# Kernel tuning notes

Measured on AMD Instinct MI355X. Metric: run time of the kernel, lower is better.

## Reference

```python
import jax, jax.numpy as jnp
import numpy as np

B, C, T, F = 64, 128, 2048, 5
ALPHA, BETA = 0.5, 0.5
N = C * F  # 640 nodes


def _spatial_adjacency():
    # |i-j| <= 3 neighbors within each frequency band block (block diagonal)
    idx = np.arange(C)
    d = np.abs(idx[:, None] - idx[None, :])
    blk = ((d <= 3) & (d > 0)).astype(np.float32)
    return jnp.asarray(np.kron(np.eye(F, dtype=np.float32), blk))


A_SPATIAL = _spatial_adjacency()  # (N, N)


def setup_inputs() -> dict:
    key = jax.random.key(0)
    ks = jax.random.split(key, 5)
    names = ['delta', 'theta', 'alpha', 'beta', 'gamma']
    return {n: jax.random.normal(k, (B, C, T), dtype=jnp.float32) for n, k in zip(names, ks)}


def _strg(delta, theta, alpha, beta, gamma):
    bands = jnp.stack([delta, theta, alpha, beta, gamma], axis=1)  # (B, F, C, T)
    Bn, Fn, Cn, Tn = bands.shape

    # bandpower = unbiased variance over time (torch.var default ddof=1)
    bp = jnp.var(bands, axis=3, ddof=1)  # (B, F, C)
    bandpowers = jnp.transpose(bp, (0, 2, 1))  # (B, C, F)
    # node ordering: node f*C + ch -> bandpowers[b, ch, f] == bp[b, f, ch]
    node_features = bp.reshape(Bn, Fn * Cn, 1)

    # Pearson-style functional connectivity per batch & band (vectorized)
    mean = jnp.mean(bands, axis=3, keepdims=True)
    std = jnp.std(bands, axis=3, ddof=1, keepdims=True)  # torch.std unbiased
    xn = (bands - mean) / (std + 1e-8)
    corr = jnp.einsum('bfct,bfdt->bfcd', xn, xn) / (Tn - 1)  # (B, F, C, C)
    corr = jnp.abs(corr)
    eye = jnp.eye(Cn, dtype=corr.dtype)
    corr = corr * (1.0 - eye) + eye  # zero diag, then set diag = 1
    corr = 0.5 * (corr + jnp.swapaxes(corr, 2, 3))

    # block-diagonal assembly into full functional adjacency
    A_func = jnp.zeros((Bn, N, N), dtype=corr.dtype)
    for f in range(Fn):
        s = f * Cn
        A_func = A_func.at[:, s:s + Cn, s:s + Cn].set(corr[:, f])

    A = ALPHA * A_SPATIAL[None] + BETA * A_func  # (B, N, N)

    # symmetric degree normalization D^-1/2 A D^-1/2
    D = jnp.sum(A, axis=2)
    d_inv_sqrt = (D + 1e-8) ** -0.5
    d_inv_sqrt = jnp.where(jnp.isinf(d_inv_sqrt), 0.0, d_inv_sqrt)
    A_norm = d_inv_sqrt[:, :, None] * A * d_inv_sqrt[:, None, :]

    return A_norm, node_features, bandpowers


def reference(delta, theta, alpha, beta, gamma):
    return _strg(delta, theta, alpha, beta, gamma)
```

## Files before the change

kernel.cpp:

```cpp
#include <hip/hip_runtime.h>
#include <hip/hip_bf16.h>

#define Bn 64
#define Cn 128
#define Tn 2048
#define Fn 5
#define Nn 640
#define TCHUNK 64
#define NCHUNK 32
#define BUFBYTES (Cn * TCHUNK * 2)

typedef __attribute__((ext_vector_type(8))) short bf16x8;
typedef __attribute__((ext_vector_type(4))) short bf16x4;
typedef __attribute__((ext_vector_type(4))) float f32x4;

__device__ __forceinline__ short f2bf(float f) {
    union { float f; unsigned u; } v; v.f = f;
    unsigned r = (v.u + 0x7fffu + ((v.u >> 16) & 1u)) >> 16;
    return (short)r;
}

__device__ __forceinline__ int swz(int row, int bytecol) {
    return (row * 128 + bytecol) ^ ((row & 7) << 4);
}

__device__ __forceinline__ const float* pick_band(const float* d0, const float* d1,
                                                  const float* d2, const float* d3,
                                                  const float* d4, int f) {
    return (f == 0) ? d0 : (f == 1) ? d1 : (f == 2) ? d2 : (f == 3) ? d3 : d4;
}

__global__ __launch_bounds__(512, 4)
void strg_mono(const float* __restrict__ d0, const float* __restrict__ d1,
               const float* __restrict__ d2, const float* __restrict__ d3,
               const float* __restrict__ d4, float* __restrict__ out)
{
    __shared__ __align__(16) char smem[Cn * Cn * 4];
    __shared__ float S_lds[Cn], diag[Cn], mrow[Cn], ivrow[Cn], Dsum[Cn], dinv_s[Cn];

    const int tid = threadIdx.x;
    const int bfid = blockIdx.x;
    const int b = bfid / Fn;
    const int f = bfid - b * Fn;
    const float* src = pick_band(d0, d1, d2, d3, d4, f) + (size_t)b * Cn * Tn;

    if (tid < Cn) { S_lds[tid] = 0.0f; Dsum[tid] = 0.0f; }

    const int srow = tid >> 4;
    const int sseg = tid & 15;
    const float* tb0 = src + (size_t)srow * Tn + sseg * 4;

    const int lane = tid & 63;
    const int w  = tid >> 6;
    const int wr = w >> 1;
    const int wc = w & 1;
    const int r0 = wr * 32;
    const int c0 = wc * 64;
    const int lg = lane >> 4;
    const int ll = lane & 15;

    f32x4 acc[2][4] = {};
    float psum[4] = {0.f, 0.f, 0.f, 0.f};
    float4 pfA[4], pfB[4];

    auto issueA = [&](int ch) {
        const float* cb = tb0 + ch * TCHUNK;
        #pragma unroll
        for (int i = 0; i < 4; ++i) pfA[i] = *(const float4*)(cb + (size_t)(i * 32) * Tn);
    };
    auto issueB = [&](int ch) {
        const float* cb = tb0 + ch * TCHUNK;
        #pragma unroll
        for (int i = 0; i < 4; ++i) pfB[i] = *(const float4*)(cb + (size_t)(i * 32) * Tn);
    };
    auto convA = [&](int buf) {
        char* base = smem + buf * BUFBYTES;
        #pragma unroll
        for (int i = 0; i < 4; ++i) {
            const int row = i * 32 + srow;
            float4 v = pfA[i];
            psum[i] += v.x + v.y + v.z + v.w;
            bf16x4 h; h[0] = f2bf(v.x); h[1] = f2bf(v.y); h[2] = f2bf(v.z); h[3] = f2bf(v.w);
            *(bf16x4*)(base + swz(row, sseg * 8)) = h;
        }
    };
    auto convB = [&](int buf) {
        char* base = smem + buf * BUFBYTES;
        #pragma unroll
        for (int i = 0; i < 4; ++i) {
            const int row = i * 32 + srow;
            float4 v = pfB[i];
            psum[i] += v.x + v.y + v.z + v.w;
            bf16x4 h; h[0] = f2bf(v.x); h[1] = f2bf(v.y); h[2] = f2bf(v.z); h[3] = f2bf(v.w);
            *(bf16x4*)(base + swz(row, sseg * 8)) = h;
        }
    };
    auto mfma_phase = [&](int buf) {
        const char* base = smem + buf * BUFBYTES;
        #pragma unroll
        for (int ks = 0; ks < 2; ++ks) {
            bf16x8 afr[2], bfr[4];
            #pragma unroll
            for (int m = 0; m < 2; ++m)
                afr[m] = *(const bf16x8*)(base + swz(r0 + m * 16 + ll, ks * 64 + lg * 16));
            #pragma unroll
            for (int n = 0; n < 4; ++n)
                bfr[n] = *(const bf16x8*)(base + swz(c0 + n * 16 + ll, ks * 64 + lg * 16));
            #pragma unroll
            for (int m = 0; m < 2; ++m)
                #pragma unroll
                for (int n = 0; n < 4; ++n)
                    acc[m][n] = __builtin_amdgcn_mfma_f32_16x16x32_bf16(afr[m], bfr[n], acc[m][n], 0, 0, 0);
        }
    };

    issueA(0);
    issueB(1);
    convA(0);
    issueA(2);
    asm volatile("s_waitcnt lgkmcnt(0)" ::: "memory");
    __builtin_amdgcn_s_barrier();
    __builtin_amdgcn_sched_barrier(0);

    for (int k = 0; k < NCHUNK; k += 2) {
        convB(1);
        if (k + 3 < NCHUNK) issueB(k + 3);
        mfma_phase(0);
        asm volatile("s_waitcnt lgkmcnt(0)" ::: "memory");
        __builtin_amdgcn_s_barrier();
        __builtin_amdgcn_sched_barrier(0);

        if (k + 2 < NCHUNK) {
            convA(0);
            if (k + 4 < NCHUNK) issueA(k + 4);
        }
        mfma_phase(1);
        asm volatile("s_waitcnt lgkmcnt(0)" ::: "memory");
        __builtin_amdgcn_s_barrier();
        __builtin_amdgcn_sched_barrier(0);
    }

    #pragma unroll
    for (int i = 0; i < 4; ++i)
        atomicAdd(&S_lds[i * 32 + srow], psum[i]);

    #pragma unroll
    for (int m = 0; m < 2; ++m)
      #pragma unroll
      for (int n = 0; n < 4; ++n)
        #pragma unroll
        for (int e = 0; e < 4; ++e) {
            const int row = r0 + m * 16 + lg * 4 + e;
            const int col = c0 + n * 16 + ll;
            if (row == col) diag[row] = acc[m][n][e];
        }
    __syncthreads();

    if (tid < Cn) {
        const float S  = S_lds[tid];
        const float mu = S * (1.0f / Tn);
        float var = (diag[tid] - (float)Tn * mu * mu) * (1.0f / (Tn - 1));
        var = var < 0.f ? 0.f : var;
        const float sd = sqrtf(var);
        mrow[tid]  = mu;
        ivrow[tid] = 1.0f / (sd + 1e-8f);
        const size_t ofs = (size_t)Bn * Nn * Nn;
        out[ofs + (size_t)b * Nn + f * Cn + tid] = var;
        out[ofs + (size_t)Bn * Nn + ((size_t)b * Cn + tid) * Fn + f] = var;
    }
    __syncthreads();

    float* At = (float*)smem;
    {
        float mi[2][4], ii[2][4], mj[4], ij[4];
        #pragma unroll
        for (int m = 0; m < 2; ++m)
          #pragma unroll
          for (int e = 0; e < 4; ++e) {
              const int row = r0 + m * 16 + lg * 4 + e;
              mi[m][e] = mrow[row];
              ii[m][e] = ivrow[row];
          }
        #pragma unroll
        for (int n = 0; n < 4; ++n) {
            const int col = c0 + n * 16 + ll;
            mj[n] = mrow[col];
            ij[n] = ivrow[col];
        }
        const float inv = 1.0f / (Tn - 1);
        #pragma unroll
        for (int m = 0; m < 2; ++m)
          #pragma unroll
          for (int e = 0; e < 4; ++e) {
              const int row = r0 + m * 16 + lg * 4 + e;
              float s = 0.f;
              #pragma unroll
              for (int n = 0; n < 4; ++n) {
                  const int col = c0 + n * 16 + ll;
                  float c = fabsf((acc[m][n][e] - (float)Tn * mi[m][e] * mj[n])
                                  * ii[m][e] * ij[n] * inv);
                  c = (row == col) ? 1.0f : c;
                  const int d = row > col ? row - col : col - row;
                  const float spa = (d >= 1 && d <= 3) ? 1.0f : 0.0f;
                  const float a = 0.5f * (spa + c);
                  At[row * Cn + col] = a;
                  s += a;
              }
              s += __shfl_xor(s, 1);
              s += __shfl_xor(s, 2);
              s += __shfl_xor(s, 4);
              s += __shfl_xor(s, 8);
              if (ll == 0) atomicAdd(&Dsum[row], s);
          }
    }
    __syncthreads();

    if (tid < Cn) dinv_s[tid] = rsqrtf(Dsum[tid] + 1e-8f);
    __syncthreads();

    float* Ob = out + (size_t)b * Nn * Nn;
    const int fc = f * Cn;
    for (int e = 0; e < 40; ++e) {
        const int idx4 = e * 2048 + tid * 4;
        const int row = idx4 / Nn;
        const int col = idx4 - row * Nn;
        const int cl = col - fc;
        float4 v = {0.f, 0.f, 0.f, 0.f};
        if (cl >= 0 && cl < Cn) {
            const float dr = dinv_s[row];
            v.x = dr * At[row * Cn + cl]     * dinv_s[cl];
            v.y = dr * At[row * Cn + cl + 1] * dinv_s[cl + 1];
            v.z = dr * At[row * Cn + cl + 2] * dinv_s[cl + 2];
            v.w = dr * At[row * Cn + cl + 3] * dinv_s[cl + 3];
        }
        *(float4*)(Ob + (size_t)(fc + row) * Nn + col) = v;
    }
}

extern "C" void kernel_launch(void* const* d_in, const int* in_sizes, int n_in,
                              void* d_out, int out_size, void* d_ws, size_t ws_size,
                              hipStream_t stream) {
    const float* d0 = (const float*)d_in[0];
    const float* d1 = (const float*)d_in[1];
    const float* d2 = (const float*)d_in[2];
    const float* d3 = (const float*)d_in[3];
    const float* d4 = (const float*)d_in[4];
    float* out = (float*)d_out;

    strg_mono<<<dim3(Bn * Fn), dim3(512), 0, stream>>>(d0, d1, d2, d3, d4, out);
}
```

Baseline: 108.6 us.

## Use 1024-thread blocks, shuffle-reduce row sums, and nontemporal output stores

Doubles the block size to 16 waves, splitting the 128x128 correlation tile into 4x4 wave tiles so each wave holds half the accumulators and loads half the prefetch rows. Per-row time sums are reduced with wave shuffles and written directly instead of LDS atomics. Output stores switch to nontemporal to avoid cache pollution on the large streamed adjacency writes. The cost is more barrier participants and higher per-CU thread pressure with only 320 blocks.

```diff
diff --git a/kernel.cpp b/kernel.cpp
--- a/kernel.cpp
+++ b/kernel.cpp
@@ -30,7 +30,7 @@
     return (f == 0) ? d0 : (f == 1) ? d1 : (f == 2) ? d2 : (f == 3) ? d3 : d4;
 }
 
-__global__ __launch_bounds__(512, 4)
+__global__ __launch_bounds__(1024, 8)
 void strg_mono(const float* __restrict__ d0, const float* __restrict__ d1,
                const float* __restrict__ d2, const float* __restrict__ d3,
                const float* __restrict__ d4, float* __restrict__ out)
@@ -52,64 +52,64 @@
 
     const int lane = tid & 63;
     const int w  = tid >> 6;
-    const int wr = w >> 1;
-    const int wc = w & 1;
+    const int wr = w >> 2;
+    const int wc = w & 3;
     const int r0 = wr * 32;
-    const int c0 = wc * 64;
+    const int c0 = wc * 32;
     const int lg = lane >> 4;
     const int ll = lane & 15;
 
-    f32x4 acc[2][4] = {};
-    float psum[4] = {0.f, 0.f, 0.f, 0.f};
-    float4 pfA[4], pfB[4];
+    f32x4 acc[2][2] = {};
+    float psum[2] = {0.f, 0.f};
+    float4 pfA[2], pfB[2];
 
     auto issueA = [&](int ch) {
         const float* cb = tb0 + ch * TCHUNK;
         #pragma unroll
-        for (int i = 0; i < 4; ++i) pfA[i] = *(const float4*)(cb + (size_t)(i * 32) * Tn);
+        for (int i = 0; i < 2; ++i) pfA[i] = *(const float4*)(cb + (size_t)(i * 64) * Tn);
     };
     auto issueB = [&](int ch) {
         const float* cb = tb0 + ch * TCHUNK;
         #pragma unroll
-        for (int i = 0; i < 4; ++i) pfB[i] = *(const float4*)(cb + (size_t)(i * 32) * Tn);
+        for (int i = 0; i < 2; ++i) pfB[i] = *(const float4*)(cb + (size_t)(i * 64) * Tn);
     };
     auto convA = [&](int buf) {
         char* base = smem + buf * BUFBYTES;
         #pragma unroll
-        for (int i = 0; i < 4; ++i) {
-            const int row = i * 32 + srow;
+        for (int i = 0; i < 2; ++i) {
+            const int row = i * 64 + srow;
             float4 v = pfA[i];
             psum[i] += v.x + v.y + v.z + v.w;
-            bf16x4 h; h[0] = f2bf(v.x); h[1] = f2bf(v.y); h[2] = f2bf(v.z); h[3] = f2bf(v.w);
-            *(bf16x4*)(base + swz(row, sseg * 8)) = h;
+            bf16x4 hh; hh[0] = f2bf(v.x); hh[1] = f2bf(v.y); hh[2] = f2bf(v.z); hh[3] = f2bf(v.w);
+            *(bf16x4*)(base + swz(row, sseg * 8)) = hh;
         }
     };
     auto convB = [&](int buf) {
         char* base = smem + buf * BUFBYTES;
         #pragma unroll
-        for (int i = 0; i < 4; ++i) {
-            const int row = i * 32 + srow;
+        for (int i = 0; i < 2; ++i) {
+            const int row = i * 64 + srow;
             float4 v = pfB[i];
             psum[i] += v.x + v.y + v.z + v.w;
-            bf16x4 h; h[0] = f2bf(v.x); h[1] = f2bf(v.y); h[2] = f2bf(v.z); h[3] = f2bf(v.w);
-            *(bf16x4*)(base + swz(row, sseg * 8)) = h;
+            bf16x4 hh; hh[0] = f2bf(v.x); hh[1] = f2bf(v.y); hh[2] = f2bf(v.z); hh[3] = f2bf(v.w);
+            *(bf16x4*)(base + swz(row, sseg * 8)) = hh;
         }
     };
     auto mfma_phase = [&](int buf) {
         const char* base = smem + buf * BUFBYTES;
         #pragma unroll
         for (int ks = 0; ks < 2; ++ks) {
-            bf16x8 afr[2], bfr[4];
+            bf16x8 afr[2], bfr[2];
             #pragma unroll
             for (int m = 0; m < 2; ++m)
                 afr[m] = *(const bf16x8*)(base + swz(r0 + m * 16 + ll, ks * 64 + lg * 16));
             #pragma unroll
-            for (int n = 0; n < 4; ++n)
+            for (int n = 0; n < 2; ++n)
                 bfr[n] = *(const bf16x8*)(base + swz(c0 + n * 16 + ll, ks * 64 + lg * 16));
             #pragma unroll
             for (int m = 0; m < 2; ++m)
                 #pragma unroll
-                for (int n = 0; n < 4; ++n)
+                for (int n = 0; n < 2; ++n)
                     acc[m][n] = __builtin_amdgcn_mfma_f32_16x16x32_bf16(afr[m], bfr[n], acc[m][n], 0, 0, 0);
         }
     };
@@ -141,13 +141,19 @@
     }
 
     #pragma unroll
-    for (int i = 0; i < 4; ++i)
-        atomicAdd(&S_lds[i * 32 + srow], psum[i]);
+    for (int i = 0; i < 2; ++i) {
+        float s = psum[i];
+        s += __shfl_xor(s, 1);
+        s += __shfl_xor(s, 2);
+        s += __shfl_xor(s, 4);
+        s += __shfl_xor(s, 8);
+        if (ll == 0) S_lds[i * 64 + srow] = s;
+    }
 
     #pragma unroll
     for (int m = 0; m < 2; ++m)
       #pragma unroll
-      for (int n = 0; n < 4; ++n)
+      for (int n = 0; n < 2; ++n)
         #pragma unroll
         for (int e = 0; e < 4; ++e) {
             const int row = r0 + m * 16 + lg * 4 + e;
@@ -165,14 +171,14 @@
         mrow[tid]  = mu;
         ivrow[tid] = 1.0f / (sd + 1e-8f);
         const size_t ofs = (size_t)Bn * Nn * Nn;
-        out[ofs + (size_t)b * Nn + f * Cn + tid] = var;
-        out[ofs + (size_t)Bn * Nn + ((size_t)b * Cn + tid) * Fn + f] = var;
+        __builtin_nontemporal_store(var, &out[ofs + (size_t)b * Nn + f * Cn + tid]);
+        __builtin_nontemporal_store(var, &out[ofs + (size_t)Bn * Nn + ((size_t)b * Cn + tid) * Fn + f]);
     }
     __syncthreads();
 
     float* At = (float*)smem;
     {
-        float mi[2][4], ii[2][4], mj[4], ij[4];
+        float mi[2][4], ii[2][4], mj[2], ij[2];
         #pragma unroll
         for (int m = 0; m < 2; ++m)
           #pragma unroll
@@ -182,7 +188,7 @@
               ii[m][e] = ivrow[row];
           }
         #pragma unroll
-        for (int n = 0; n < 4; ++n) {
+        for (int n = 0; n < 2; ++n) {
             const int col = c0 + n * 16 + ll;
             mj[n] = mrow[col];
             ij[n] = ivrow[col];
@@ -195,7 +201,7 @@
               const int row = r0 + m * 16 + lg * 4 + e;
               float s = 0.f;
               #pragma unroll
-              for (int n = 0; n < 4; ++n) {
+              for (int n = 0; n < 2; ++n) {
                   const int col = c0 + n * 16 + ll;
                   float c = fabsf((acc[m][n][e] - (float)Tn * mi[m][e] * mj[n])
                                   * ii[m][e] * ij[n] * inv);
@@ -220,20 +226,20 @@
 
     float* Ob = out + (size_t)b * Nn * Nn;
     const int fc = f * Cn;
-    for (int e = 0; e < 40; ++e) {
-        const int idx4 = e * 2048 + tid * 4;
+    for (int e = 0; e < 20; ++e) {
+        const int idx4 = e * 4096 + tid * 4;
         const int row = idx4 / Nn;
         const int col = idx4 - row * Nn;
         const int cl = col - fc;
-        float4 v = {0.f, 0.f, 0.f, 0.f};
+        f32x4 v = {0.f, 0.f, 0.f, 0.f};
         if (cl >= 0 && cl < Cn) {
             const float dr = dinv_s[row];
-            v.x = dr * At[row * Cn + cl]     * dinv_s[cl];
-            v.y = dr * At[row * Cn + cl + 1] * dinv_s[cl + 1];
-            v.z = dr * At[row * Cn + cl + 2] * dinv_s[cl + 2];
-            v.w = dr * At[row * Cn + cl + 3] * dinv_s[cl + 3];
-        }
-        *(float4*)(Ob + (size_t)(fc + row) * Nn + col) = v;
+            v[0] = dr * At[row * Cn + cl]     * dinv_s[cl];
+            v[1] = dr * At[row * Cn + cl + 1] * dinv_s[cl + 1];
+            v[2] = dr * At[row * Cn + cl + 2] * dinv_s[cl + 2];
+            v[3] = dr * At[row * Cn + cl + 3] * dinv_s[cl + 3];
+        }
+        __builtin_nontemporal_store(v, (f32x4*)(Ob + (size_t)(fc + row) * Nn + col));
     }
 }
 
@@ -247,5 +253,5 @@
     const float* d4 = (const float*)d_in[4];
     float* out = (float*)d_out;
 
-    strg_mono<<<dim3(Bn * Fn), dim3(512), 0, stream>>>(d0, d1, d2, d3, d4, out);
-}
+    strg_mono<<<dim3(Bn * Fn), dim3(1024), 0, stream>>>(d0, d1, d2, d3, d4, out);
+}
```

After: 113.7 us. 1.05x slower.

## Overlap zero-fill of off-diagonal blocks with MFMA loop using nontemporal stores

Applied to the files above, without the earlier changes.

Moves the zero writes for the off-diagonal parts of each 128x640 output row slab into the main correlation loop, one 512-thread float4 batch per chunk, so they overlap with loads and MFMA work. The epilogue then writes only the 128x128 diagonal block. All output stores become nontemporal to avoid polluting cache. This adds store traffic to the memory system during the input-streaming phase, which may contend with the global loads.

```diff
diff --git a/kernel.cpp b/kernel.cpp
--- a/kernel.cpp
+++ b/kernel.cpp
@@ -59,6 +59,10 @@
     const int lg = lane >> 4;
     const int ll = lane & 15;
 
+    float* Ob = out + (size_t)b * Nn * Nn;
+    const int fc  = f * Cn;
+    const int fc4 = f * 32;
+
     f32x4 acc[2][4] = {};
     float psum[4] = {0.f, 0.f, 0.f, 0.f};
     float4 pfA[4], pfB[4];
@@ -80,8 +84,8 @@
             const int row = i * 32 + srow;
             float4 v = pfA[i];
             psum[i] += v.x + v.y + v.z + v.w;
-            bf16x4 h; h[0] = f2bf(v.x); h[1] = f2bf(v.y); h[2] = f2bf(v.z); h[3] = f2bf(v.w);
-            *(bf16x4*)(base + swz(row, sseg * 8)) = h;
+            bf16x4 hh; hh[0] = f2bf(v.x); hh[1] = f2bf(v.y); hh[2] = f2bf(v.z); hh[3] = f2bf(v.w);
+            *(bf16x4*)(base + swz(row, sseg * 8)) = hh;
         }
     };
     auto convB = [&](int buf) {
@@ -91,8 +95,8 @@
             const int row = i * 32 + srow;
             float4 v = pfB[i];
             psum[i] += v.x + v.y + v.z + v.w;
-            bf16x4 h; h[0] = f2bf(v.x); h[1] = f2bf(v.y); h[2] = f2bf(v.z); h[3] = f2bf(v.w);
-            *(bf16x4*)(base + swz(row, sseg * 8)) = h;
+            bf16x4 hh; hh[0] = f2bf(v.x); hh[1] = f2bf(v.y); hh[2] = f2bf(v.z); hh[3] = f2bf(v.w);
+            *(bf16x4*)(base + swz(row, sseg * 8)) = hh;
         }
     };
     auto mfma_phase = [&](int buf) {
@@ -113,6 +117,14 @@
                     acc[m][n] = __builtin_amdgcn_mfma_f32_16x16x32_bf16(afr[m], bfr[n], acc[m][n], 0, 0, 0);
         }
     };
+    auto zstore = [&](int j) {
+        const int zidx = j * 512 + tid;
+        const int row = zidx >> 7;
+        const int v   = zidx & 127;
+        const int col4 = (v < fc4) ? v : (v + 32);
+        const f32x4 z = {0.f, 0.f, 0.f, 0.f};
+        __builtin_nontemporal_store(z, (f32x4*)(Ob + (size_t)(fc + row) * Nn + col4 * 4));
+    };
 
     issueA(0);
     issueB(1);
@@ -126,6 +138,7 @@
         convB(1);
         if (k + 3 < NCHUNK) issueB(k + 3);
         mfma_phase(0);
+        zstore(k);
         asm volatile("s_waitcnt lgkmcnt(0)" ::: "memory");
         __builtin_amdgcn_s_barrier();
         __builtin_amdgcn_sched_barrier(0);
@@ -135,6 +148,7 @@
             if (k + 4 < NCHUNK) issueA(k + 4);
         }
         mfma_phase(1);
+        zstore(k + 1);
         asm volatile("s_waitcnt lgkmcnt(0)" ::: "memory");
         __builtin_amdgcn_s_barrier();
         __builtin_amdgcn_sched_barrier(0);
@@ -165,8 +179,8 @@
         mrow[tid]  = mu;
         ivrow[tid] = 1.0f / (sd + 1e-8f);
         const size_t ofs = (size_t)Bn * Nn * Nn;
-        out[ofs + (size_t)b * Nn + f * Cn + tid] = var;
-        out[ofs + (size_t)Bn * Nn + ((size_t)b * Cn + tid) * Fn + f] = var;
+        __builtin_nontemporal_store(var, &out[ofs + (size_t)b * Nn + f * Cn + tid]);
+        __builtin_nontemporal_store(var, &out[ofs + (size_t)Bn * Nn + ((size_t)b * Cn + tid) * Fn + f]);
     }
     __syncthreads();
 
@@ -218,22 +232,18 @@
     if (tid < Cn) dinv_s[tid] = rsqrtf(Dsum[tid] + 1e-8f);
     __syncthreads();
 
-    float* Ob = out + (size_t)b * Nn * Nn;
-    const int fc = f * Cn;
-    for (int e = 0; e < 40; ++e) {
-        const int idx4 = e * 2048 + tid * 4;
-        const int row = idx4 / Nn;
-        const int col = idx4 - row * Nn;
-        const int cl = col - fc;
-        float4 v = {0.f, 0.f, 0.f, 0.f};
-        if (cl >= 0 && cl < Cn) {
-            const float dr = dinv_s[row];
-            v.x = dr * At[row * Cn + cl]     * dinv_s[cl];
-            v.y = dr * At[row * Cn + cl + 1] * dinv_s[cl + 1];
-            v.z = dr * At[row * Cn + cl + 2] * dinv_s[cl + 2];
-            v.w = dr * At[row * Cn + cl + 3] * dinv_s[cl + 3];
-        }
-        *(float4*)(Ob + (size_t)(fc + row) * Nn + col) = v;
+    for (int e = 0; e < 8; ++e) {
+        const int idx4 = e * 512 + tid;
+        const int row = idx4 >> 5;
+        const int c4  = idx4 & 31;
+        const int cl  = c4 * 4;
+        const float dr = dinv_s[row];
+        f32x4 v;
+        v[0] = dr * At[row * Cn + cl]     * dinv_s[cl];
+        v[1] = dr * At[row * Cn + cl + 1] * dinv_s[cl + 1];
+        v[2] = dr * At[row * Cn + cl + 2] * dinv_s[cl + 2];
+        v[3] = dr * At[row * Cn + cl + 3] * dinv_s[cl + 3];
+        __builtin_nontemporal_store(v, (f32x4*)(Ob + (size_t)(fc + row) * Nn + fc + cl));
     }
 }
 
```

Measured after the change: 130.9 us. 20.6% more time.
